# Kernel optimization log

Measured on AMD Instinct MI355X. Metric: run time of the kernel, lower is better.

Reference implementation:

```python
import jax, jax.numpy as jnp
import numpy as np

# AnyPrecision bit-plane packing convention (documented, since the CUDA kernel's
# exact bit order is an implementation detail):
#  - qweight[b, o, w] is an int32 word holding bit-plane b for output channel o,
#    covering input features i = 32*w .. 32*w+31, LSB-first within the word.
#  - plane 0 is the least-significant bit of the w_bits-wide LUT index.
#  - dequantized weight[o, i] = lut[o, index(o, i)].

IN_FEATURES = 4096
OUT_FEATURES = 4096
MAX_BITS = 8
W_BITS = 4


def anyprec_dequant(qweight, lut, w_bits):
    """qweight: (max_bits, O, In//32) int32; lut: (O, 2**w_bits). Returns (O, In)."""
    O, W = qweight.shape[1], qweight.shape[2]
    shifts = jnp.arange(32, dtype=jnp.int32)  # LSB-first within each word
    # (w_bits, O, W, 32): bit of each weight at each plane
    bits = (qweight[:w_bits, :, :, None] >> shifts) & 1
    plane_weights = (jnp.int32(1) << jnp.arange(w_bits, dtype=jnp.int32))[:, None, None, None]
    idx = jnp.sum(bits * plane_weights, axis=0).reshape(O, W * 32)  # (O, In) LUT indices
    return jnp.take_along_axis(lut, idx, axis=1)  # (O, In)


def setup_inputs() -> dict:
    key = jax.random.key(0)
    k1, k2, k3, k4 = jax.random.split(key, 4)
    x = jax.random.normal(k1, (4, 2048, IN_FEATURES), dtype=jnp.float32)
    qweight = jax.random.randint(
        k2, (MAX_BITS, OUT_FEATURES, IN_FEATURES // 32), 0, 2147483647, dtype=jnp.int32)
    lut = jax.random.normal(k3, (OUT_FEATURES, 2 ** W_BITS), dtype=jnp.float32) * 0.05
    bias = jax.random.normal(k4, (OUT_FEATURES,), dtype=jnp.float32) * 0.02
    return {"x": x, "qweight": qweight, "lut": lut, "bias": bias, "w_bits": W_BITS}


def reference(x, qweight, lut, bias, w_bits):
    # GEMM path of AnyPrecisionLinear.forward (B*T > 1)
    weight = anyprec_dequant(qweight, lut, w_bits)         # (O, In)
    y = jnp.einsum('bti,oi->bto', x, weight)               # (B, T, O)
    return y + bias
```

## Files before the change

### kernel.cpp

```cpp
#include <hip/hip_runtime.h>
#include <hip/hip_bf16.h>
#include <stdint.h>

#define M_DIM 8192
#define N_DIM 4096
#define K_DIM 4096

typedef __attribute__((ext_vector_type(4))) float f32x4;
typedef __attribute__((ext_vector_type(4))) int   i32x4;

#define GLD_LDS16(gaddr, laddr)                                            \
  __builtin_amdgcn_global_load_lds(                                        \
      (const __attribute__((address_space(1))) uint32_t*)(gaddr),          \
      (__attribute__((address_space(3))) uint32_t*)(laddr), 16, 0, 0)


__global__ __launch_bounds__(256) void prep_kernel(
    const int* __restrict__ q, const float* __restrict__ lut,
    signed char* __restrict__ Wq, float* __restrict__ sw,
    const float* __restrict__ x, signed char* __restrict__ Xq,
    float* __restrict__ sxd) {
  __shared__ char sm[16384];
  const int b = blockIdx.x;
  const int tid = threadIdx.x;
  if (b < 2048) {
    const int ob = b >> 4, wb = b & 15;
    const int o_l = tid >> 3, w_l = tid & 7;
    const int o = ob * 32 + o_l;
    const int PLANE = N_DIM * (K_DIM / 32);
    const int base = o * (K_DIM / 32) + wb * 8 + w_l;
    uint32_t q0 = (uint32_t)q[base];
    uint32_t q1 = (uint32_t)q[PLANE + base];
    uint32_t q2 = (uint32_t)q[2 * PLANE + base];
    uint32_t q3 = (uint32_t)q[3 * PLANE + base];
    const float* lrow = lut + o * 16;
    float lmax = 1e-30f;
#pragma unroll
    for (int j = 0; j < 16; ++j) lmax = fmaxf(lmax, fabsf(lrow[j]));
    const float qs = 127.0f / lmax;
    signed char l8[16];
#pragma unroll
    for (int j = 0; j < 16; ++j)
      l8[j] = (signed char)(int)rintf(lrow[j] * qs);
    if (wb == 0 && w_l == 0) sw[o] = lmax * (1.0f / 127.0f);

    union { i32x4 v; signed char c[16]; } u0, u1;
#pragma unroll
    for (int i = 0; i < 16; ++i) {
      uint32_t idx = ((q0 >> i) & 1u) | (((q1 >> i) & 1u) << 1) |
                     (((q2 >> i) & 1u) << 2) | (((q3 >> i) & 1u) << 3);
      u0.c[i] = l8[idx];
    }
#pragma unroll
    for (int i = 16; i < 32; ++i) {
      uint32_t idx = ((q0 >> i) & 1u) | (((q1 >> i) & 1u) << 1) |
                     (((q2 >> i) & 1u) << 2) | (((q3 >> i) & 1u) << 3);
      u1.c[i - 16] = l8[idx];
    }
    const int t_local = w_l >> 1;
    const int f_local = o_l >> 4;
    const int kc0 = (w_l & 1) * 2;
    char* sp = sm + t_local * 2048 + f_local * 1024;
    *(i32x4*)(sp + ((o_l & 15) + kc0 * 16) * 16)       = u0.v;
    *(i32x4*)(sp + ((o_l & 15) + (kc0 + 1) * 16) * 16) = u1.v;
    __syncthreads();
    const int rp = ob >> 3, h = (ob >> 2) & 1, f0 = (ob * 2) & 7;
#pragma unroll
    for (int c = 0; c < 2; ++c) {
      const int ci = c * 256 + tid;
      const int t_loc = ci >> 7, off = ci & 127;
      const size_t outb = (size_t)(rp * 64 + wb * 4 + t_loc) * 16384
                          + h * 8192 + f0 * 1024 + off * 16;
      *(i32x4*)(Wq + outb) = *(i32x4*)(sm + t_loc * 2048 + off * 16);
    }
  } else {
    const int r = b - 2048;
    const float* xr = x + (size_t)r * K_DIM;
    float v[16];
#pragma unroll
    for (int s = 0; s < 4; ++s) {
      f32x4 u = *(const f32x4*)(xr + tid * 4 + s * 1024);
      v[s * 4 + 0] = u[0]; v[s * 4 + 1] = u[1];
      v[s * 4 + 2] = u[2]; v[s * 4 + 3] = u[3];
    }
    float m = 0.0f;
#pragma unroll
    for (int i = 0; i < 16; ++i) m = fmaxf(m, fabsf(v[i]));
#pragma unroll
    for (int off = 32; off; off >>= 1) m = fmaxf(m, __shfl_down(m, off));
    float* red = (float*)(sm + 8192);
    if ((tid & 63) == 0) red[tid >> 6] = m;
    __syncthreads();
    float rmax = fmaxf(fmaxf(red[0], red[1]), fmaxf(red[2], red[3]));
    rmax = fmaxf(rmax, 1e-30f);
    if (tid == 0) sxd[r] = rmax * (1.0f / 127.0f);
    const float qs = 127.0f / rmax;
#pragma unroll
    for (int s = 0; s < 4; ++s) {
      int qi[4];
#pragma unroll
      for (int j = 0; j < 4; ++j) {
        float qc = fminf(127.0f, fmaxf(-127.0f, rintf(v[s * 4 + j] * qs)));
        qi[j] = (int)qc;
      }
      uint32_t w = (qi[0] & 255) | ((qi[1] & 255) << 8) |
                   ((qi[2] & 255) << 16) | ((uint32_t)(qi[3] & 255) << 24);
      *(uint32_t*)(sm + tid * 4 + s * 1024) = w;
    }
    __syncthreads();
    const int rp = r >> 8, h = (r >> 7) & 1, f = (r >> 4) & 7;
    const int kt = tid >> 2, kc = tid & 3;
    const size_t outb = (size_t)(rp * 64 + kt) * 16384 + h * 8192
                        + f * 1024 + ((r & 15) + kc * 16) * 16;
    *(i32x4*)(Xq + outb) = *(i32x4*)(sm + tid * 16);
  }
}

__global__ __launch_bounds__(512, 2) void anyprec_gemm_kernel(
    const signed char* __restrict__ A,
    const signed char* __restrict__ B,
    const float* __restrict__ sxd, const float* __restrict__ sw,
    const float* __restrict__ bias,
    float* __restrict__ C) {
  __shared__ char lds[4][32768];

  int bid = blockIdx.x;
  int swz = (bid & 7) * 64 + (bid >> 3);
  int mb = swz >> 4;
  int nb = swz & 15;

  const int tid  = threadIdx.x;
  const int lane = tid & 63;
  const int wid  = tid >> 6;
  const int wr   = wid >> 2;
  const int wc   = wid & 3;
  const int tid16  = tid * 16;
  const int lane16 = lane * 16;

  char* lbase = &lds[0][0];

  const char* gA = (const char*)A + (size_t)mb * 1048576;
  const char* gB = (const char*)B + (size_t)nb * 1048576;

  i32x4 acc[2][2][4][2];
#pragma unroll
  for (int qm = 0; qm < 2; ++qm)
#pragma unroll
    for (int qn = 0; qn < 2; ++qn)
#pragma unroll
      for (int mf = 0; mf < 4; ++mf)
#pragma unroll
        for (int nf = 0; nf < 2; ++nf) acc[qm][qn][mf][nf] = (i32x4)0;

  i32x4 a0[4], a1[4], b0[2], b1[2];

#define STAGE_T(t, rb) {                                                   \
    char* lb_ = lbase + (rb) * 32768 + tid16;                              \
    const char* ga_ = gA + (size_t)(t) * 16384 + tid16;                    \
    const char* gb_ = gB + (size_t)(t) * 16384 + tid16;                    \
    GLD_LDS16(ga_,        lb_);                                            \
    GLD_LDS16(ga_ + 8192, lb_ + 8192);                                     \
    GLD_LDS16(gb_,        lb_ + 16384);                                    \
    GLD_LDS16(gb_ + 8192, lb_ + 24576); }

#define LDA(dst, qm, rb) {                                                 \
    const char* p_ = lbase + (rb) * 32768 + (qm) * 8192 + wr * 4096        \
                     + lane16;                                             \
    _Pragma("unroll")                                                      \
    for (int mf = 0; mf < 4; ++mf)                                         \
      dst[mf] = *(const i32x4*)(p_ + mf * 1024); }

#define LDB(dst, qn, rb) {                                                 \
    const char* p_ = lbase + (rb) * 32768 + 16384 + (qn) * 8192            \
                     + wc * 2048 + lane16;                                 \
    _Pragma("unroll")                                                      \
    for (int nf = 0; nf < 2; ++nf)                                         \
      dst[nf] = *(const i32x4*)(p_ + nf * 1024); }

#define MMA(qm, qn, aa, bb) {                                              \
    _Pragma("unroll")                                                      \
    for (int mf = 0; mf < 4; ++mf)                                         \
      _Pragma("unroll")                                                    \
      for (int nf = 0; nf < 2; ++nf)                                       \
        acc[qm][qn][mf][nf] = __builtin_amdgcn_mfma_i32_16x16x64_i8(       \
            aa[mf], bb[nf], acc[qm][qn][mf][nf], 0, 0, 0); }

#define PRIO1 __builtin_amdgcn_s_setprio(1);
#define PRIO0 __builtin_amdgcn_s_setprio(0);
#define BAR   __builtin_amdgcn_s_barrier();
#define LGKM0 asm volatile("s_waitcnt lgkmcnt(0)" ::: "memory");
#define VMC(n) asm volatile("s_waitcnt vmcnt(" #n ")" ::: "memory");

#define PHASE_BODY(rb)                                                     \
    LDA(a0, 0, rb); LDB(b0, 0, rb); LDB(b1, 1, rb); LDA(a1, 1, rb);        \
    PRIO1;                                                                 \
    MMA(0, 0, a0, b0); MMA(0, 1, a0, b1);                                  \
    MMA(1, 1, a1, b1); MMA(1, 0, a1, b0);                                  \
    PRIO0;

  STAGE_T(0, 0);
  STAGE_T(1, 1);
  STAGE_T(2, 2);
  VMC(8); BAR;

  for (int t = 0; t < 61; ++t) {
    const int rb = t & 3;
    STAGE_T(t + 3, (t + 3) & 3);
    PHASE_BODY(rb);
    LGKM0;
    VMC(8);
    BAR;
  }
  PHASE_BODY(1);
  LGKM0; VMC(4); BAR;
  PHASE_BODY(2);
  LGKM0; VMC(0); BAR;
  PHASE_BODY(3);

  const int cL = lane & 15;
  const int rL = (lane >> 4) * 4;
#pragma unroll
  for (int qn = 0; qn < 2; ++qn)
#pragma unroll
    for (int nf = 0; nf < 2; ++nf) {
      int col = nb * 256 + qn * 128 + wc * 32 + nf * 16 + cL;
      float bv  = bias[col];
      float swc = sw[col];
#pragma unroll
      for (int qm = 0; qm < 2; ++qm)
#pragma unroll
        for (int mf = 0; mf < 4; ++mf) {
          int row0 = mb * 256 + qm * 128 + wr * 64 + mf * 16 + rL;
#pragma unroll
          for (int j = 0; j < 4; ++j) {
            int row = row0 + j;
            float s = sxd[row] * swc;
            C[(size_t)row * N_DIM + col] =
                fmaf((float)acc[qm][qn][mf][nf][j], s, bv);
          }
        }
    }
#undef STAGE_T
#undef LDA
#undef LDB
#undef MMA
#undef PRIO1
#undef PRIO0
#undef BAR
#undef LGKM0
#undef VMC
#undef PHASE_BODY
}

extern "C" void kernel_launch(void* const* d_in, const int* in_sizes, int n_in,
                              void* d_out, int out_size, void* d_ws, size_t ws_size,
                              hipStream_t stream) {
  const float* x    = (const float*)d_in[0];
  const int*   qw   = (const int*)d_in[1];
  const float* lut  = (const float*)d_in[2];
  const float* bias = (const float*)d_in[3];

  char* wsb = (char*)d_ws;
  signed char* Wq  = (signed char*)wsb;
  signed char* Xq  = (signed char*)(wsb + (size_t)16 * 1024 * 1024);
  float*       sxd = (float*)(wsb + (size_t)48 * 1024 * 1024);
  float*       sw  = sxd + M_DIM;

  {
    prep_kernel<<<10240, 256, 0, stream>>>(qw, lut, Wq, sw, x, Xq, sxd);
  }
  {
    dim3 grid((M_DIM / 256) * (N_DIM / 256));
    anyprec_gemm_kernel<<<grid, 512, 0, stream>>>(Xq, Wq, sxd, sw, bias,
                                                  (float*)d_out);
  }
}
```

Before: 194.7 us.

## Software-pipeline LDS fragment loads across MFMA groups into the next k-tile

Restructures the GEMM main loop so that the A and B register fragments for the next k-tile are read from LDS while MFMAs on the current fragments execute, rather than loading all fragments up front before each compute phase. The global-load wait count is tightened to match the deeper prefetch, and the epilogue is unrolled by hand to drain the pipeline. The goal is to hide LDS read latency behind matrix-core work. In exchange it holds more fragment registers live, and the tighter vmcnt waits may stall earlier on global staging.

```diff
diff --git a/kernel.cpp b/kernel.cpp
--- a/kernel.cpp
+++ b/kernel.cpp
@@ -191,31 +191,52 @@
 #define LGKM0 asm volatile("s_waitcnt lgkmcnt(0)" ::: "memory");
 #define VMC(n) asm volatile("s_waitcnt vmcnt(" #n ")" ::: "memory");
 
-#define PHASE_BODY(rb)                                                     \
-    LDA(a0, 0, rb); LDB(b0, 0, rb); LDB(b1, 1, rb); LDA(a1, 1, rb);        \
-    PRIO1;                                                                 \
-    MMA(0, 0, a0, b0); MMA(0, 1, a0, b1);                                  \
-    MMA(1, 1, a1, b1); MMA(1, 0, a1, b0);                                  \
-    PRIO0;
-
   STAGE_T(0, 0);
   STAGE_T(1, 1);
   STAGE_T(2, 2);
-  VMC(8); BAR;
+  VMC(4); BAR;
+  LDA(a0, 0, 0); LDB(b0, 0, 0); LDB(b1, 1, 0);
 
   for (int t = 0; t < 61; ++t) {
-    const int rb = t & 3;
+    const int rb = t & 3, rn = (t + 1) & 3;
     STAGE_T(t + 3, (t + 3) & 3);
-    PHASE_BODY(rb);
+    PRIO1;
+    LDA(a1, 1, rb);
+    MMA(0, 0, a0, b0); MMA(0, 1, a0, b1);
+    LDA(a0, 0, rn);
+    MMA(1, 1, a1, b1); LDB(b1, 1, rn);
+    MMA(1, 0, a1, b0); LDB(b0, 0, rn);
+    PRIO0;
     LGKM0;
-    VMC(8);
+    VMC(4);
     BAR;
   }
-  PHASE_BODY(1);
-  LGKM0; VMC(4); BAR;
-  PHASE_BODY(2);
-  LGKM0; VMC(0); BAR;
-  PHASE_BODY(3);
+  {
+    PRIO1;
+    LDA(a1, 1, 1);
+    MMA(0, 0, a0, b0); MMA(0, 1, a0, b1);
+    LDA(a0, 0, 2);
+    MMA(1, 1, a1, b1); LDB(b1, 1, 2);
+    MMA(1, 0, a1, b0); LDB(b0, 0, 2);
+    PRIO0;
+    LGKM0; VMC(0); BAR;
+  }
+  {
+    PRIO1;
+    LDA(a1, 1, 2);
+    MMA(0, 0, a0, b0); MMA(0, 1, a0, b1);
+    LDA(a0, 0, 3);
+    MMA(1, 1, a1, b1); LDB(b1, 1, 3);
+    MMA(1, 0, a1, b0); LDB(b0, 0, 3);
+    PRIO0;
+  }
+  {
+    PRIO1;
+    LDA(a1, 1, 3);
+    MMA(0, 0, a0, b0); MMA(0, 1, a0, b1);
+    MMA(1, 1, a1, b1); MMA(1, 0, a1, b0);
+    PRIO0;
+  }
 
   const int cL = lane & 15;
   const int rL = (lane >> 4) * 4;
@@ -249,7 +270,6 @@
 #undef BAR
 #undef LGKM0
 #undef VMC
-#undef PHASE_BODY
 }
 
 extern "C" void kernel_launch(void* const* d_in, const int* in_sizes, int n_in,
```

Result: no change. 195.9 us (+0.7%).
